# Kernel tuning notes

Measured on AMD Instinct MI355X. Metric: run time of the kernel, lower is better.

The kernel has to match this reference:

```python
import jax, jax.numpy as jnp
import numpy as np

N, E = 50000, 800000
IN, HID, OUT = 128, 128, 64
BN_EPS = 1e-5


def _w(key, fan_in, fan_out):
    return jax.random.normal(key, (fan_in, fan_out), dtype=jnp.float32) / np.sqrt(fan_in)


def setup_inputs() -> dict:
    key = jax.random.key(0)
    ks = jax.random.split(key, 12)
    x = jax.random.normal(ks[0], (N, IN), dtype=jnp.float32)
    src = jax.random.randint(ks[1], (E,), 0, N, dtype=jnp.int32)
    dst = jax.random.randint(ks[2], (E,), 0, N, dtype=jnp.int32)
    eps = jax.random.normal(ks[3], (N, OUT), dtype=jnp.float32)
    return {
        "x": x, "src": src, "dst": dst, "eps": eps,
        # SAGEConv 1: in -> hidden (lin_l has bias, lin_r no bias, mean aggr)
        "W1l": _w(ks[4], IN, HID), "W1r": _w(ks[5], IN, HID), "b1": jnp.zeros((HID,), jnp.float32),
        "g1": jnp.ones((HID,), jnp.float32), "be1": jnp.zeros((HID,), jnp.float32),
        # SAGEConv 2: hidden -> 2*hidden
        "W2l": _w(ks[6], HID, 2 * HID), "W2r": _w(ks[7], HID, 2 * HID), "b2": jnp.zeros((2 * HID,), jnp.float32),
        "g2": jnp.ones((2 * HID,), jnp.float32), "be2": jnp.zeros((2 * HID,), jnp.float32),
        # SAGEConv 3: 2*hidden -> 2*out
        "W3l": _w(ks[8], 2 * HID, 2 * OUT), "W3r": _w(ks[9], 2 * HID, 2 * OUT), "b3": jnp.zeros((2 * OUT,), jnp.float32),
    }


def _sage(h, src, dst, Wl, Wr, b):
    # mean-aggregate source features at destination nodes, then two GEMMs
    msg = jax.ops.segment_sum(h[src], dst, num_segments=N)          # [N, F]
    deg = jax.ops.segment_sum(jnp.ones((src.shape[0],), h.dtype), dst, num_segments=N)
    aggr = msg / jnp.maximum(deg, 1.0)[:, None]
    return aggr @ Wl + h @ Wr + b


def _bn(h, gamma, beta):
    m = jnp.mean(h, axis=0)
    v = jnp.var(h, axis=0)
    return gamma * (h - m) * jax.lax.rsqrt(v + BN_EPS) + beta


def reference(x, src, dst, eps, W1l, W1r, b1, g1, be1, W2l, W2r, b2, g2, be2, W3l, W3r, b3):
    h = jax.nn.relu(_sage(x, src, dst, W1l, W1r, b1))
    h = _bn(h, g1, be1)                       # dropout = identity (eval)
    h = jax.nn.relu(_sage(h, src, dst, W2l, W2r, b2))
    h = _bn(h, g2, be2)
    h = _sage(h, src, dst, W3l, W3r, b3)      # [N, 2*OUT]
    mean, log_std = jnp.split(h, 2, axis=-1)
    z = mean + jnp.exp(log_std) * eps         # reparameterize
    return z
```

## Files before the change

kernel.cpp:

```cpp
#include <hip/hip_runtime.h>
#include <math.h>

#define N_NODES 50000
#define N_EDGES 800000
#define BN_EPS_F 1e-5f
#define SCAN_BS 512
#define SCAN_NB 98
#define GXP 392

typedef unsigned short ushort_t;
typedef unsigned int uint_t;
typedef __attribute__((ext_vector_type(8))) short bf16x8;
typedef __attribute__((ext_vector_type(4))) float f32x4;

static __device__ __forceinline__ float4 ld4(const float* p) {
    return *reinterpret_cast<const float4*>(p);
}
static __device__ __forceinline__ float bf2f(ushort_t u) {
    return __uint_as_float(((uint_t)u) << 16);
}
static __device__ __forceinline__ ushort_t f2b(float f) {
    uint_t u = __float_as_uint(f);
    u += 0x7fffu + ((u >> 16) & 1u);
    return (ushort_t)(u >> 16);
}
static __device__ __forceinline__ void gload16(const void* g, void* l) {
    __builtin_amdgcn_global_load_lds(
        (const __attribute__((address_space(1))) void*)g,
        (__attribute__((address_space(3))) void*)l, 16, 0, 0);
}


__global__ void k_zero_i32(int* __restrict__ p, int n) {
    int i = blockIdx.x * blockDim.x + threadIdx.x;
    if (i < n) p[i] = 0;
}

__global__ void k_pre(const int* __restrict__ dst, int* __restrict__ deg,
                      ushort_t* __restrict__ rank,
                      const float* __restrict__ x, ushort_t* __restrict__ xb,
                      const float* __restrict__ W1l, const float* __restrict__ W1r,
                      const float* __restrict__ W2l, ushort_t* __restrict__ wt1l,
                      ushort_t* __restrict__ wt1r, ushort_t* __restrict__ wt2l) {
    int b = blockIdx.x;
    if (b < 6250) {
        int role = b & 1;
        int id = (b >> 1) * 256 + threadIdx.x;
        if (role == 0) {
            rank[id] = (ushort_t)atomicAdd(&deg[dst[id]], 1);
        } else {
            float4 a = ld4(x + (size_t)id * 8);
            float4 c = ld4(x + (size_t)id * 8 + 4);
            uint_t o0 = (uint_t)f2b(a.x) | ((uint_t)f2b(a.y) << 16);
            uint_t o1 = (uint_t)f2b(a.z) | ((uint_t)f2b(a.w) << 16);
            uint_t o2 = (uint_t)f2b(c.x) | ((uint_t)f2b(c.y) << 16);
            uint_t o3 = (uint_t)f2b(c.z) | ((uint_t)f2b(c.w) << 16);
            *reinterpret_cast<uint4*>(xb + (size_t)id * 8) = make_uint4(o0, o1, o2, o3);
        }
    } else {
        int idx = (b - 6250) * 256 + threadIdx.x;
        if (idx < 16384) {
            int f = idx >> 7, k = idx & 127;
            wt1l[idx] = f2b(W1l[(size_t)k * 128 + f]);
        } else if (idx < 32768) {
            int j = idx - 16384;
            int f = j >> 7, k = j & 127;
            wt1r[j] = f2b(W1r[(size_t)k * 128 + f]);
        } else {
            int j = idx - 32768;
            int f = j >> 7, k = j & 127;
            wt2l[j] = f2b(W2l[(size_t)k * 256 + f]);
        }
    }
}

__global__ void k_scan1(const int* __restrict__ deg, int* __restrict__ offs, int* __restrict__ bsum) {
    __shared__ int sh[SCAN_BS];
    int t = threadIdx.x;
    int g = blockIdx.x * SCAN_BS + t;
    int v = (g < N_NODES) ? deg[g] : 0;
    sh[t] = v;
    __syncthreads();
    for (int off = 1; off < SCAN_BS; off <<= 1) {
        int add = (t >= off) ? sh[t - off] : 0;
        __syncthreads();
        sh[t] += add;
        __syncthreads();
    }
    if (g < N_NODES) offs[g] = sh[t] - v;
    if (t == SCAN_BS - 1) bsum[blockIdx.x] = sh[t];
}

__global__ void k_scan2(int* __restrict__ bsum, int nb) {
    __shared__ int sh[128];
    int t = threadIdx.x;
    int v = (t < nb) ? bsum[t] : 0;
    sh[t] = v;
    __syncthreads();
    for (int off = 1; off < 128; off <<= 1) {
        int add = (t >= off) ? sh[t - off] : 0;
        __syncthreads();
        sh[t] += add;
        __syncthreads();
    }
    if (t < nb) bsum[t] = sh[t] - v;
}

__global__ void k_scan3(const int* __restrict__ deg, int* __restrict__ offs,
                        const int* __restrict__ bsum, float* __restrict__ inv_deg) {
    int g = blockIdx.x * blockDim.x + threadIdx.x;
    if (g < N_NODES) {
        offs[g] += bsum[g / SCAN_BS];
        int d = deg[g];
        inv_deg[g] = 1.0f / (float)(d > 1 ? d : 1);
    }
}

__global__ void k_fill2(const int* __restrict__ src, const int* __restrict__ dst,
                        const int* __restrict__ offs, const ushort_t* __restrict__ rank,
                        ushort_t* __restrict__ eids) {
    int e = blockIdx.x * blockDim.x + threadIdx.x;
    if (e < N_EDGES) eids[offs[dst[e]] + (int)rank[e]] = (ushort_t)src[e];
}


__global__ void k_prep2(const float* __restrict__ W2r, const float* __restrict__ b2,
                        const float* __restrict__ scsh1, ushort_t* __restrict__ wt2r,
                        float* __restrict__ bias2) {
    int bid = blockIdx.x;
    if (bid < 128) {
        int idx = bid * 256 + threadIdx.x;
        int f = idx >> 7, k = idx & 127;
        wt2r[idx] = f2b(scsh1[k] * W2r[(size_t)k * 256 + f]);
    } else {
        int f = threadIdx.x;
        float s = b2[f];
        for (int k = 0; k < 128; ++k) s += scsh1[128 + k] * W2r[(size_t)k * 256 + f];
        bias2[f] = s;
    }
}

__global__ void k_prep3(const float* __restrict__ W3l, const float* __restrict__ W3r,
                        const float* __restrict__ b3, const float* __restrict__ scsh2,
                        ushort_t* __restrict__ wt3l, ushort_t* __restrict__ wt3r,
                        float* __restrict__ bias3l, float* __restrict__ bias3r) {
    int bid = blockIdx.x;
    if (bid < 256) {
        int half = bid >> 7;
        int idx = (bid & 127) * 256 + threadIdx.x;
        int f = idx >> 8, k = idx & 255;
        const float* W = half ? W3r : W3l;
        ushort_t* WT = half ? wt3r : wt3l;
        WT[idx] = f2b(scsh2[k] * W[(size_t)k * 128 + f]);
    } else {
        int t = threadIdx.x;
        int f = t & 127;
        const float* W = (t < 128) ? W3l : W3r;
        float s = (t < 128) ? 0.f : b3[f];
        for (int k = 0; k < 256; ++k) s += scsh2[256 + k] * W[(size_t)k * 128 + f];
        float* out = (t < 128) ? bias3l : bias3r;
        out[f] = s;
    }
}


#define ACCUM8(a) do { \
    acc[0] += bf2f((ushort_t)(a).x); acc[1] += bf2f((ushort_t)((a).x >> 16)); \
    acc[2] += bf2f((ushort_t)(a).y); acc[3] += bf2f((ushort_t)((a).y >> 16)); \
    acc[4] += bf2f((ushort_t)(a).z); acc[5] += bf2f((ushort_t)((a).z >> 16)); \
    acc[6] += bf2f((ushort_t)(a).w); acc[7] += bf2f((ushort_t)((a).w >> 16)); } while (0)

static __device__ __forceinline__ void gather_rows(
        const ushort_t* __restrict__ h, const ushort_t* __restrict__ eids,
        int beg, int d, int g, size_t coff, float* acc) {
    int j = 0;
    for (; j + 32 <= d; j += 32) {
        int s[8];
#pragma unroll
        for (int k = 0; k < 8; ++k) s[k] = eids[beg + j + k * 4 + g];
        uint4 a[8];
#pragma unroll
        for (int k = 0; k < 8; ++k) a[k] = *reinterpret_cast<const uint4*>(h + (size_t)s[k] * 128 + coff);
#pragma unroll
        for (int k = 0; k < 8; ++k) ACCUM8(a[k]);
    }
    for (; j + 16 <= d; j += 16) {
        int s[4];
#pragma unroll
        for (int k = 0; k < 4; ++k) s[k] = eids[beg + j + k * 4 + g];
        uint4 a[4];
#pragma unroll
        for (int k = 0; k < 4; ++k) a[k] = *reinterpret_cast<const uint4*>(h + (size_t)s[k] * 128 + coff);
#pragma unroll
        for (int k = 0; k < 4; ++k) ACCUM8(a[k]);
    }
    for (; j + 8 <= d; j += 8) {
        int s0 = eids[beg + j + g];
        int s1 = eids[beg + j + 4 + g];
        uint4 a = *reinterpret_cast<const uint4*>(h + (size_t)s0 * 128 + coff);
        uint4 b = *reinterpret_cast<const uint4*>(h + (size_t)s1 * 128 + coff);
        ACCUM8(a); ACCUM8(b);
    }
    for (; j < d; j += 4) {
        int e = j + g;
        if (e < d) {
            int s0 = eids[beg + e];
            uint4 a = *reinterpret_cast<const uint4*>(h + (size_t)s0 * 128 + coff);
            ACCUM8(a);
        }
    }
}

template<int BN>
__global__ __launch_bounds__(256) void k_agg16(
        const ushort_t* __restrict__ h, const ushort_t* __restrict__ eids,
        const int* __restrict__ offs, const int* __restrict__ deg,
        const float* __restrict__ inv_deg, const float* __restrict__ scsh,
        ushort_t* __restrict__ out) {
    int node = (blockIdx.x * 256 + threadIdx.x) >> 6;
    int lane = threadIdx.x & 63;
    if (node >= N_NODES) return;
    const int g = lane >> 4;
    const int lr = lane & 15;
    float acc[8];
#pragma unroll
    for (int v = 0; v < 8; ++v) acc[v] = 0.f;
    const int beg = offs[node];
    const int d = deg[node];
    const size_t coff = (size_t)lr * 8;
    gather_rows(h, eids, beg, d, g, coff, acc);
#pragma unroll
    for (int v = 0; v < 8; ++v) acc[v] += __shfl_xor(acc[v], 16);
#pragma unroll
    for (int v = 0; v < 8; ++v) acc[v] += __shfl_xor(acc[v], 32);

    if (g == 0) {
        float sc = inv_deg[node];
        if (BN) {
            float4 sa0 = ld4(&scsh[lr * 8]), sa1 = ld4(&scsh[lr * 8 + 4]);
            float4 sb0 = ld4(&scsh[128 + lr * 8]), sb1 = ld4(&scsh[128 + lr * 8 + 4]);
            if (d > 0) {
                acc[0] = acc[0] * sc * sa0.x + sb0.x; acc[1] = acc[1] * sc * sa0.y + sb0.y;
                acc[2] = acc[2] * sc * sa0.z + sb0.z; acc[3] = acc[3] * sc * sa0.w + sb0.w;
                acc[4] = acc[4] * sc * sa1.x + sb1.x; acc[5] = acc[5] * sc * sa1.y + sb1.y;
                acc[6] = acc[6] * sc * sa1.z + sb1.z; acc[7] = acc[7] * sc * sa1.w + sb1.w;
            } else {
#pragma unroll
                for (int v = 0; v < 8; ++v) acc[v] = 0.f;
            }
        } else {
#pragma unroll
            for (int v = 0; v < 8; ++v) acc[v] *= sc;
        }
        uint4 o;
        o.x = (uint_t)f2b(acc[0]) | ((uint_t)f2b(acc[1]) << 16);
        o.y = (uint_t)f2b(acc[2]) | ((uint_t)f2b(acc[3]) << 16);
        o.z = (uint_t)f2b(acc[4]) | ((uint_t)f2b(acc[5]) << 16);
        o.w = (uint_t)f2b(acc[6]) | ((uint_t)f2b(acc[7]) << 16);
        *reinterpret_cast<uint4*>(out + (size_t)node * 128 + coff) = o;
    }
}

__global__ __launch_bounds__(256) void k_agg_reparam(
        const ushort_t* __restrict__ t3, const ushort_t* __restrict__ eids,
        const int* __restrict__ offs, const int* __restrict__ deg,
        const float* __restrict__ inv_deg, const float* __restrict__ u,
        const float* __restrict__ eps, float* __restrict__ z) {
    int node = (blockIdx.x * 256 + threadIdx.x) >> 6;
    int lane = threadIdx.x & 63;
    if (node >= N_NODES) return;
    const int g = lane >> 4;
    const int lr = lane & 15;
    float acc[8];
#pragma unroll
    for (int v = 0; v < 8; ++v) acc[v] = 0.f;
    const int beg = offs[node];
    const int d = deg[node];
    const size_t coff = (size_t)lr * 8;
    gather_rows(t3, eids, beg, d, g, coff, acc);
#pragma unroll
    for (int v = 0; v < 8; ++v) acc[v] += __shfl_xor(acc[v], 16);
#pragma unroll
    for (int v = 0; v < 8; ++v) acc[v] += __shfl_xor(acc[v], 32);
    float ls[8];
#pragma unroll
    for (int v = 0; v < 8; ++v) ls[v] = __shfl_down(acc[v], 8);

    if (g == 0 && lr < 8) {
        float sc = inv_deg[node];
        const float* um = u + (size_t)node * 128 + lr * 8;
        const float* ul = u + (size_t)node * 128 + 64 + lr * 8;
        const float* ep = eps + (size_t)node * 64 + lr * 8;
        float4 um0 = ld4(um), um1 = ld4(um + 4);
        float4 ul0 = ld4(ul), ul1 = ld4(ul + 4);
        float4 e0 = ld4(ep), e1 = ld4(ep + 4);
        float4 o0, o1;
        o0.x = (acc[0] * sc + um0.x) + expf(ls[0] * sc + ul0.x) * e0.x;
        o0.y = (acc[1] * sc + um0.y) + expf(ls[1] * sc + ul0.y) * e0.y;
        o0.z = (acc[2] * sc + um0.z) + expf(ls[2] * sc + ul0.z) * e0.z;
        o0.w = (acc[3] * sc + um0.w) + expf(ls[3] * sc + ul0.w) * e0.w;
        o1.x = (acc[4] * sc + um1.x) + expf(ls[4] * sc + ul1.x) * e1.x;
        o1.y = (acc[5] * sc + um1.y) + expf(ls[5] * sc + ul1.y) * e1.y;
        o1.z = (acc[6] * sc + um1.z) + expf(ls[6] * sc + ul1.z) * e1.z;
        o1.w = (acc[7] * sc + um1.w) + expf(ls[7] * sc + ul1.w) * e1.w;
        float* zp = z + (size_t)node * 64 + lr * 8;
        *reinterpret_cast<float4*>(zp) = o0;
        *reinterpret_cast<float4*>(zp + 4) = o1;
    }
}


template<int RELU, int OUTB, int DUAL, int BIAS, int STATS, int SELY>
__global__ __launch_bounds__(256) void k_gemm_mfma(
        const ushort_t* __restrict__ A1, const ushort_t* __restrict__ A2,
        const ushort_t* __restrict__ B1, const ushort_t* __restrict__ B2,
        const float* __restrict__ bias, void* __restrict__ out,
        int K, int F, float* __restrict__ partials,
        const float* __restrict__ bias2, void* __restrict__ out2) {
    __shared__ __align__(16) short lds[8192];
    const int tid = threadIdx.x;
    const int lane = tid & 63;
    const int w = tid >> 6;
    const int row0 = blockIdx.x * 128;
    const int col0 = SELY ? 0 : blockIdx.y * 128;
    const int wr = (w >> 1) * 64;
    const int wc = (w & 1) * 64;

    const ushort_t* __restrict__ B0 = (SELY && blockIdx.y) ? B2 : B1;
    const float* __restrict__ biasp = (SELY && blockIdx.y) ? bias2 : bias;
    void* __restrict__ outp = (SELY && blockIdx.y) ? out2 : out;
    const bool outb = SELY ? (blockIdx.y == 0) : (OUTB != 0);

    int rowA[2], slA[2];
#pragma unroll
    for (int p = 0; p < 2; ++p) {
        int c = (p * 4 + w) * 64 + lane;
        int r = c >> 2, sp = c & 3;
        rowA[p] = r;
        slA[p] = sp ^ ((r >> 1) & 3);
    }
    const int q = lane >> 4, lr = lane & 15;
    int aoff[4], boff[4];
#pragma unroll
    for (int f = 0; f < 4; ++f) {
        int ra = wr + f * 16 + lr;
        aoff[f] = ra * 32 + (q ^ ((ra >> 1) & 3)) * 8;
        int rb = wc + f * 16 + lr;
        boff[f] = 4096 + rb * 32 + (q ^ ((rb >> 1) & 3)) * 8;
    }

    f32x4 acc[4][4];
#pragma unroll
    for (int mf = 0; mf < 4; ++mf)
#pragma unroll
        for (int nf = 0; nf < 4; ++nf)
            acc[mf][nf] = (f32x4){0.f, 0.f, 0.f, 0.f};

    for (int m = 0; m < (DUAL ? 2 : 1); ++m) {
        const ushort_t* __restrict__ A = m ? A2 : A1;
        const ushort_t* __restrict__ B = m ? B2 : B0;
        for (int k0 = 0; k0 < K; k0 += 32) {
            __syncthreads();
#pragma unroll
            for (int p = 0; p < 2; ++p) {
                int gr = row0 + rowA[p];
                if (gr > N_NODES - 1) gr = N_NODES - 1;
                gload16(A + (size_t)gr * K + k0 + slA[p] * 8, &lds[(p * 4 + w) * 512]);
                int gc = col0 + rowA[p];
                gload16(B + (size_t)gc * K + k0 + slA[p] * 8, &lds[4096 + (p * 4 + w) * 512]);
            }
            asm volatile("s_waitcnt vmcnt(0)" ::: "memory");
            __syncthreads();
            bf16x8 av[4], bv[4];
#pragma unroll
            for (int f = 0; f < 4; ++f) {
                av[f] = *reinterpret_cast<const bf16x8*>(&lds[aoff[f]]);
                bv[f] = *reinterpret_cast<const bf16x8*>(&lds[boff[f]]);
            }
#pragma unroll
            for (int mf = 0; mf < 4; ++mf)
#pragma unroll
                for (int nf = 0; nf < 4; ++nf)
                    acc[mf][nf] = __builtin_amdgcn_mfma_f32_16x16x32_bf16(
                        av[mf], bv[nf], acc[mf][nf], 0, 0, 0);
        }
    }

    const int orow = row0 + wr + q * 4;
    const int ocol = col0 + wc + lr;
    float s[4], s2[4];
#pragma unroll
    for (int nf = 0; nf < 4; ++nf) { s[nf] = 0.f; s2[nf] = 0.f; }
#pragma unroll
    for (int nf = 0; nf < 4; ++nf) {
        int colg = ocol + nf * 16;
        float bvs = BIAS ? biasp[colg] : 0.f;
#pragma unroll
        for (int mf = 0; mf < 4; ++mf) {
#pragma unroll
            for (int b = 0; b < 4; ++b) {
                int r = orow + mf * 16 + b;
                if (r < N_NODES) {
                    float v = acc[mf][nf][b] + bvs;
                    if (RELU) v = fmaxf(v, 0.f);
                    if (STATS) { s[nf] += v; s2[nf] += v * v; }
                    if (outb)
                        ((ushort_t*)outp)[(size_t)r * F + colg] = f2b(v);
                    else
                        ((float*)outp)[(size_t)r * F + colg] = v;
                }
            }
        }
    }

    if constexpr (STATS) {
        __syncthreads();
        float* sdf = (float*)lds;
        const int u = (w >> 1) * 4 + q;
#pragma unroll
        for (int nf = 0; nf < 4; ++nf) {
            int cb = wc + nf * 16 + lr;
            sdf[u * 128 + cb] = s[nf];
            sdf[1024 + u * 128 + cb] = s2[nf];
        }
        __syncthreads();
        if (tid < 128) {
            float ss = 0.f, qq = 0.f;
#pragma unroll
            for (int u2 = 0; u2 < 8; ++u2) {
                ss += sdf[u2 * 128 + tid];
                qq += sdf[1024 + u2 * 128 + tid];
            }
            int cg = col0 + tid;
            partials[(size_t)cg * GXP + blockIdx.x] = ss;
            partials[(size_t)(F + cg) * GXP + blockIdx.x] = qq;
        }
    }
}


template<int F>
__global__ __launch_bounds__(64) void k_bn_scsh(
        const float* __restrict__ partials, const float* __restrict__ gamma,
        const float* __restrict__ beta, float* __restrict__ scsh, int GX) {
    const int c = blockIdx.x;
    const int l = threadIdx.x;
    float s = 0.f, q2 = 0.f;
    for (int g = l; g < GX; g += 64) {
        s += partials[(size_t)c * GXP + g];
        q2 += partials[(size_t)(F + c) * GXP + g];
    }
#pragma unroll
    for (int off = 1; off < 64; off <<= 1) {
        s += __shfl_xor(s, off);
        q2 += __shfl_xor(q2, off);
    }
    if (l == 0) {
        float mean = s * (1.0f / N_NODES);
        float var = q2 * (1.0f / N_NODES) - mean * mean;
        float sc = gamma[c] * rsqrtf(var + BN_EPS_F);
        scsh[c] = sc;
        scsh[F + c] = beta[c] - mean * sc;
    }
}


extern "C" void kernel_launch(void* const* d_in, const int* in_sizes, int n_in,
                              void* d_out, int out_size, void* d_ws, size_t ws_size,
                              hipStream_t stream) {
    (void)in_sizes; (void)n_in; (void)out_size; (void)ws_size;
    const float* x   = (const float*)d_in[0];
    const int*   src = (const int*)d_in[1];
    const int*   dst = (const int*)d_in[2];
    const float* eps = (const float*)d_in[3];
    const float* W1l = (const float*)d_in[4];
    const float* W1r = (const float*)d_in[5];
    const float* b1  = (const float*)d_in[6];
    const float* g1  = (const float*)d_in[7];
    const float* be1 = (const float*)d_in[8];
    const float* W2l = (const float*)d_in[9];
    const float* W2r = (const float*)d_in[10];
    const float* b2  = (const float*)d_in[11];
    const float* g2  = (const float*)d_in[12];
    const float* be2 = (const float*)d_in[13];
    const float* W3l = (const float*)d_in[14];
    const float* W3r = (const float*)d_in[15];
    const float* b3  = (const float*)d_in[16];
    float* z = (float*)d_out;

    char* ws = (char*)d_ws;
    size_t off = 0;
    auto alloc = [&](size_t bytes) -> char* {
        char* p = ws + off;
        off += (bytes + 255) & ~(size_t)255;
        return p;
    };
    int*      deg    = (int*)alloc(N_NODES * 4);
    size_t zero_bytes = off;
    ushort_t* rank   = (ushort_t*)alloc((size_t)N_EDGES * 2);
    ushort_t* eids   = (ushort_t*)alloc((size_t)N_EDGES * 2);
    float*    scshs  = (float*)alloc(1024 * 4);
    float*    biases = (float*)alloc(512 * 4);
    int*      offs   = (int*)alloc(N_NODES * 4);
    int*      bsum   = (int*)alloc(128 * 4);
    float*    invd   = (float*)alloc(N_NODES * 4);
    ushort_t* xb     = (ushort_t*)alloc((size_t)N_NODES * 128 * 2);
    ushort_t* h1b    = (ushort_t*)alloc((size_t)N_NODES * 128 * 2);
    ushort_t* h2b    = (ushort_t*)alloc((size_t)N_NODES * 256 * 2);
    ushort_t* aggrb  = (ushort_t*)alloc((size_t)N_NODES * 256 * 2);
    float*    u3f    = (float*)alloc((size_t)N_NODES * 128 * 4);
    float*    parts  = (float*)alloc((size_t)512 * GXP * 4);
    ushort_t* wt1l   = (ushort_t*)alloc(128 * 128 * 2);
    ushort_t* wt1r   = (ushort_t*)alloc(128 * 128 * 2);
    ushort_t* wt2l   = (ushort_t*)alloc(256 * 128 * 2);
    ushort_t* wt2r   = (ushort_t*)alloc(256 * 128 * 2);
    ushort_t* wt3l   = (ushort_t*)alloc(128 * 256 * 2);
    ushort_t* wt3r   = (ushort_t*)alloc(128 * 256 * 2);
    ushort_t* t3b    = aggrb;

    float* scsh1  = scshs;
    float* scsh2  = scshs + 256;
    float* bias2  = biases;
    float* bias3l = biases + 256;
    float* bias3r = biases + 384;

    k_zero_i32<<<((int)(zero_bytes / 4) + 255) / 256, 256, 0, stream>>>((int*)ws, (int)(zero_bytes / 4));
    k_pre<<<6506, 256, 0, stream>>>(dst, deg, rank, x, xb, W1l, W1r, W2l, wt1l, wt1r, wt2l);
    k_scan1<<<SCAN_NB, SCAN_BS, 0, stream>>>(deg, offs, bsum);
    k_scan2<<<1, 128, 0, stream>>>(bsum, SCAN_NB);
    k_scan3<<<(N_NODES + 255) / 256, 256, 0, stream>>>(deg, offs, bsum, invd);
    k_fill2<<<(N_EDGES + 255) / 256, 256, 0, stream>>>(src, dst, offs, rank, eids);

    const int AGG_BLKS = (N_NODES + 3) / 4;
    const int GX = (N_NODES + 127) / 128;

    k_agg16<0><<<AGG_BLKS, 256, 0, stream>>>(xb, eids, offs, deg, invd, nullptr, aggrb);
    k_gemm_mfma<1, 1, 1, 1, 1, 0><<<dim3(GX, 1), 256, 0, stream>>>(aggrb, xb, wt1l, wt1r, b1, h1b, 128, 128, parts, nullptr, nullptr);
    k_bn_scsh<128><<<128, 64, 0, stream>>>(parts, g1, be1, scsh1, GX);

    k_prep2<<<129, 256, 0, stream>>>(W2r, b2, scsh1, wt2r, bias2);
    k_agg16<1><<<AGG_BLKS, 256, 0, stream>>>(h1b, eids, offs, deg, invd, scsh1, aggrb);
    k_gemm_mfma<1, 1, 1, 1, 1, 0><<<dim3(GX, 2), 256, 0, stream>>>(aggrb, h1b, wt2l, wt2r, bias2, h2b, 128, 256, parts, nullptr, nullptr);
    k_bn_scsh<256><<<256, 64, 0, stream>>>(parts, g2, be2, scsh2, GX);

    k_prep3<<<257, 256, 0, stream>>>(W3l, W3r, b3, scsh2, wt3l, wt3r, bias3l, bias3r);
    k_gemm_mfma<0, 1, 0, 1, 0, 1><<<dim3(GX, 2), 256, 0, stream>>>(h2b, nullptr, wt3l, wt3r, bias3l, t3b, 256, 128, nullptr, bias3r, u3f);
    k_agg_reparam<<<AGG_BLKS, 256, 0, stream>>>(t3b, eids, offs, deg, invd, u3f, eps, z);
}
```

Baseline: 269.9 us.

## Gather one node per 16-lane group and store root term as bf16

```diff
diff --git a/kernel.cpp b/kernel.cpp
--- a/kernel.cpp
+++ b/kernel.cpp
@@ -170,44 +170,41 @@
     acc[4] += bf2f((ushort_t)(a).z); acc[5] += bf2f((ushort_t)((a).z >> 16)); \
     acc[6] += bf2f((ushort_t)(a).w); acc[7] += bf2f((ushort_t)((a).w >> 16)); } while (0)
 
-static __device__ __forceinline__ void gather_rows(
+static __device__ __forceinline__ void gather_rows_g(
         const ushort_t* __restrict__ h, const ushort_t* __restrict__ eids,
-        int beg, int d, int g, size_t coff, float* acc) {
+        int beg, int d, size_t coff, float* acc) {
     int j = 0;
-    for (; j + 32 <= d; j += 32) {
-        int s[8];
-#pragma unroll
-        for (int k = 0; k < 8; ++k) s[k] = eids[beg + j + k * 4 + g];
+    for (; j + 8 <= d; j += 8) {
         uint4 a[8];
 #pragma unroll
-        for (int k = 0; k < 8; ++k) a[k] = *reinterpret_cast<const uint4*>(h + (size_t)s[k] * 128 + coff);
+        for (int k = 0; k < 8; ++k) {
+            int s = eids[beg + j + k];
+            a[k] = *reinterpret_cast<const uint4*>(h + (size_t)s * 128 + coff);
+        }
 #pragma unroll
         for (int k = 0; k < 8; ++k) ACCUM8(a[k]);
     }
-    for (; j + 16 <= d; j += 16) {
-        int s[4];
-#pragma unroll
-        for (int k = 0; k < 4; ++k) s[k] = eids[beg + j + k * 4 + g];
+    for (; j + 4 <= d; j += 4) {
         uint4 a[4];
 #pragma unroll
-        for (int k = 0; k < 4; ++k) a[k] = *reinterpret_cast<const uint4*>(h + (size_t)s[k] * 128 + coff);
+        for (int k = 0; k < 4; ++k) {
+            int s = eids[beg + j + k];
+            a[k] = *reinterpret_cast<const uint4*>(h + (size_t)s * 128 + coff);
+        }
 #pragma unroll
         for (int k = 0; k < 4; ++k) ACCUM8(a[k]);
     }
-    for (; j + 8 <= d; j += 8) {
-        int s0 = eids[beg + j + g];
-        int s1 = eids[beg + j + 4 + g];
+    for (; j + 2 <= d; j += 2) {
+        int s0 = eids[beg + j];
+        int s1 = eids[beg + j + 1];
         uint4 a = *reinterpret_cast<const uint4*>(h + (size_t)s0 * 128 + coff);
         uint4 b = *reinterpret_cast<const uint4*>(h + (size_t)s1 * 128 + coff);
         ACCUM8(a); ACCUM8(b);
     }
-    for (; j < d; j += 4) {
-        int e = j + g;
-        if (e < d) {
-            int s0 = eids[beg + e];
-            uint4 a = *reinterpret_cast<const uint4*>(h + (size_t)s0 * 128 + coff);
-            ACCUM8(a);
-        }
+    if (j < d) {
+        int s0 = eids[beg + j];
+        uint4 a = *reinterpret_cast<const uint4*>(h + (size_t)s0 * 128 + coff);
+        ACCUM8(a);
     }
 }
 
@@ -217,92 +214,85 @@
         const int* __restrict__ offs, const int* __restrict__ deg,
         const float* __restrict__ inv_deg, const float* __restrict__ scsh,
         ushort_t* __restrict__ out) {
-    int node = (blockIdx.x * 256 + threadIdx.x) >> 6;
-    int lane = threadIdx.x & 63;
+    const int node = blockIdx.x * 16 + (threadIdx.x >> 4);
+    const int lr = threadIdx.x & 15;
     if (node >= N_NODES) return;
-    const int g = lane >> 4;
-    const int lr = lane & 15;
     float acc[8];
 #pragma unroll
     for (int v = 0; v < 8; ++v) acc[v] = 0.f;
     const int beg = offs[node];
     const int d = deg[node];
     const size_t coff = (size_t)lr * 8;
-    gather_rows(h, eids, beg, d, g, coff, acc);
-#pragma unroll
-    for (int v = 0; v < 8; ++v) acc[v] += __shfl_xor(acc[v], 16);
-#pragma unroll
-    for (int v = 0; v < 8; ++v) acc[v] += __shfl_xor(acc[v], 32);
-
-    if (g == 0) {
-        float sc = inv_deg[node];
-        if (BN) {
-            float4 sa0 = ld4(&scsh[lr * 8]), sa1 = ld4(&scsh[lr * 8 + 4]);
-            float4 sb0 = ld4(&scsh[128 + lr * 8]), sb1 = ld4(&scsh[128 + lr * 8 + 4]);
-            if (d > 0) {
-                acc[0] = acc[0] * sc * sa0.x + sb0.x; acc[1] = acc[1] * sc * sa0.y + sb0.y;
-                acc[2] = acc[2] * sc * sa0.z + sb0.z; acc[3] = acc[3] * sc * sa0.w + sb0.w;
-                acc[4] = acc[4] * sc * sa1.x + sb1.x; acc[5] = acc[5] * sc * sa1.y + sb1.y;
-                acc[6] = acc[6] * sc * sa1.z + sb1.z; acc[7] = acc[7] * sc * sa1.w + sb1.w;
-            } else {
-#pragma unroll
-                for (int v = 0; v < 8; ++v) acc[v] = 0.f;
-            }
+    gather_rows_g(h, eids, beg, d, coff, acc);
+
+    float sc = inv_deg[node];
+    if (BN) {
+        float4 sa0 = ld4(&scsh[lr * 8]), sa1 = ld4(&scsh[lr * 8 + 4]);
+        float4 sb0 = ld4(&scsh[128 + lr * 8]), sb1 = ld4(&scsh[128 + lr * 8 + 4]);
+        if (d > 0) {
+            acc[0] = acc[0] * sc * sa0.x + sb0.x; acc[1] = acc[1] * sc * sa0.y + sb0.y;
+            acc[2] = acc[2] * sc * sa0.z + sb0.z; acc[3] = acc[3] * sc * sa0.w + sb0.w;
+            acc[4] = acc[4] * sc * sa1.x + sb1.x; acc[5] = acc[5] * sc * sa1.y + sb1.y;
+            acc[6] = acc[6] * sc * sa1.z + sb1.z; acc[7] = acc[7] * sc * sa1.w + sb1.w;
         } else {
 #pragma unroll
-            for (int v = 0; v < 8; ++v) acc[v] *= sc;
-        }
-        uint4 o;
-        o.x = (uint_t)f2b(acc[0]) | ((uint_t)f2b(acc[1]) << 16);
-        o.y = (uint_t)f2b(acc[2]) | ((uint_t)f2b(acc[3]) << 16);
-        o.z = (uint_t)f2b(acc[4]) | ((uint_t)f2b(acc[5]) << 16);
-        o.w = (uint_t)f2b(acc[6]) | ((uint_t)f2b(acc[7]) << 16);
-        *reinterpret_cast<uint4*>(out + (size_t)node * 128 + coff) = o;
-    }
+            for (int v = 0; v < 8; ++v) acc[v] = 0.f;
+        }
+    } else {
+#pragma unroll
+        for (int v = 0; v < 8; ++v) acc[v] *= sc;
+    }
+    uint4 o;
+    o.x = (uint_t)f2b(acc[0]) | ((uint_t)f2b(acc[1]) << 16);
+    o.y = (uint_t)f2b(acc[2]) | ((uint_t)f2b(acc[3]) << 16);
+    o.z = (uint_t)f2b(acc[4]) | ((uint_t)f2b(acc[5]) << 16);
+    o.w = (uint_t)f2b(acc[6]) | ((uint_t)f2b(acc[7]) << 16);
+    *reinterpret_cast<uint4*>(out + (size_t)node * 128 + coff) = o;
 }
 
 __global__ __launch_bounds__(256) void k_agg_reparam(
         const ushort_t* __restrict__ t3, const ushort_t* __restrict__ eids,
         const int* __restrict__ offs, const int* __restrict__ deg,
-        const float* __restrict__ inv_deg, const float* __restrict__ u,
+        const float* __restrict__ inv_deg, const ushort_t* __restrict__ u,
         const float* __restrict__ eps, float* __restrict__ z) {
-    int node = (blockIdx.x * 256 + threadIdx.x) >> 6;
-    int lane = threadIdx.x & 63;
+    const int node = blockIdx.x * 16 + (threadIdx.x >> 4);
+    const int lr = threadIdx.x & 15;
     if (node >= N_NODES) return;
-    const int g = lane >> 4;
-    const int lr = lane & 15;
     float acc[8];
 #pragma unroll
     for (int v = 0; v < 8; ++v) acc[v] = 0.f;
     const int beg = offs[node];
     const int d = deg[node];
     const size_t coff = (size_t)lr * 8;
-    gather_rows(t3, eids, beg, d, g, coff, acc);
-#pragma unroll
-    for (int v = 0; v < 8; ++v) acc[v] += __shfl_xor(acc[v], 16);
-#pragma unroll
-    for (int v = 0; v < 8; ++v) acc[v] += __shfl_xor(acc[v], 32);
+    gather_rows_g(t3, eids, beg, d, coff, acc);
     float ls[8];
 #pragma unroll
     for (int v = 0; v < 8; ++v) ls[v] = __shfl_down(acc[v], 8);
 
-    if (g == 0 && lr < 8) {
+    if (lr < 8) {
         float sc = inv_deg[node];
-        const float* um = u + (size_t)node * 128 + lr * 8;
-        const float* ul = u + (size_t)node * 128 + 64 + lr * 8;
+        uint4 um4 = *reinterpret_cast<const uint4*>(u + (size_t)node * 128 + lr * 8);
+        uint4 ul4 = *reinterpret_cast<const uint4*>(u + (size_t)node * 128 + 64 + lr * 8);
         const float* ep = eps + (size_t)node * 64 + lr * 8;
-        float4 um0 = ld4(um), um1 = ld4(um + 4);
-        float4 ul0 = ld4(ul), ul1 = ld4(ul + 4);
         float4 e0 = ld4(ep), e1 = ld4(ep + 4);
+        float um[8], ul[8];
+        um[0] = bf2f((ushort_t)um4.x); um[1] = bf2f((ushort_t)(um4.x >> 16));
+        um[2] = bf2f((ushort_t)um4.y); um[3] = bf2f((ushort_t)(um4.y >> 16));
+        um[4] = bf2f((ushort_t)um4.z); um[5] = bf2f((ushort_t)(um4.z >> 16));
+        um[6] = bf2f((ushort_t)um4.w); um[7] = bf2f((ushort_t)(um4.w >> 16));
+        ul[0] = bf2f((ushort_t)ul4.x); ul[1] = bf2f((ushort_t)(ul4.x >> 16));
+        ul[2] = bf2f((ushort_t)ul4.y); ul[3] = bf2f((ushort_t)(ul4.y >> 16));
+        ul[4] = bf2f((ushort_t)ul4.z); ul[5] = bf2f((ushort_t)(ul4.z >> 16));
+        ul[6] = bf2f((ushort_t)ul4.w); ul[7] = bf2f((ushort_t)(ul4.w >> 16));
         float4 o0, o1;
-        o0.x = (acc[0] * sc + um0.x) + expf(ls[0] * sc + ul0.x) * e0.x;
-        o0.y = (acc[1] * sc + um0.y) + expf(ls[1] * sc + ul0.y) * e0.y;
-        o0.z = (acc[2] * sc + um0.z) + expf(ls[2] * sc + ul0.z) * e0.z;
-        o0.w = (acc[3] * sc + um0.w) + expf(ls[3] * sc + ul0.w) * e0.w;
-        o1.x = (acc[4] * sc + um1.x) + expf(ls[4] * sc + ul1.x) * e1.x;
-        o1.y = (acc[5] * sc + um1.y) + expf(ls[5] * sc + ul1.y) * e1.y;
-        o1.z = (acc[6] * sc + um1.z) + expf(ls[6] * sc + ul1.z) * e1.z;
-        o1.w = (acc[7] * sc + um1.w) + expf(ls[7] * sc + ul1.w) * e1.w;
+        o0.x = (acc[0] * sc + um[0]) + expf(ls[0] * sc + ul[0]) * e0.x;
+        o0.y = (acc[1] * sc + um[1]) + expf(ls[1] * sc + ul[1]) * e0.y;
+        o0.z = (acc[2] * sc + um[2]) + expf(ls[2] * sc + ul[2]) * e0.z;
+        o0.w = (acc[3] * sc + um[3]) + expf(ls[3] * sc + ul[3]) * e0.w;
+        o1.x = (acc[4] * sc + um[4]) + expf(ls[4] * sc + ul[4]) * e1.x;
+        o1.y = (acc[5] * sc + um[5]) + expf(ls[5] * sc + ul[5]) * e1.y;
+        o1.z = (acc[6] * sc + um[6]) + expf(ls[6] * sc + ul[6]) * e1.z;
+        o1.w = (acc[7] * sc + um[7]) + expf(ls[7] * sc + ul[7]) * e1.w;
         float* zp = z + (size_t)node * 64 + lr * 8;
         *reinterpret_cast<float4*>(zp) = o0;
         *reinterpret_cast<float4*>(zp + 4) = o1;
@@ -329,7 +319,6 @@
     const ushort_t* __restrict__ B0 = (SELY && blockIdx.y) ? B2 : B1;
     const float* __restrict__ biasp = (SELY && blockIdx.y) ? bias2 : bias;
     void* __restrict__ outp = (SELY && blockIdx.y) ? out2 : out;
-    const bool outb = SELY ? (blockIdx.y == 0) : (OUTB != 0);
 
     int rowA[2], slA[2];
 #pragma unroll
@@ -404,7 +393,7 @@
                     float v = acc[mf][nf][b] + bvs;
                     if (RELU) v = fmaxf(v, 0.f);
                     if (STATS) { s[nf] += v; s2[nf] += v * v; }
-                    if (outb)
+                    if (OUTB)
                         ((ushort_t*)outp)[(size_t)r * F + colg] = f2b(v);
                     else
                         ((float*)outp)[(size_t)r * F + colg] = v;
@@ -508,7 +497,7 @@
     ushort_t* h1b    = (ushort_t*)alloc((size_t)N_NODES * 128 * 2);
     ushort_t* h2b    = (ushort_t*)alloc((size_t)N_NODES * 256 * 2);
     ushort_t* aggrb  = (ushort_t*)alloc((size_t)N_NODES * 256 * 2);
-    float*    u3f    = (float*)alloc((size_t)N_NODES * 128 * 4);
+    ushort_t* u3b    = (ushort_t*)alloc((size_t)N_NODES * 128 * 2);
     float*    parts  = (float*)alloc((size_t)512 * GXP * 4);
     ushort_t* wt1l   = (ushort_t*)alloc(128 * 128 * 2);
     ushort_t* wt1r   = (ushort_t*)alloc(128 * 128 * 2);
@@ -531,7 +520,7 @@
     k_scan3<<<(N_NODES + 255) / 256, 256, 0, stream>>>(deg, offs, bsum, invd);
     k_fill2<<<(N_EDGES + 255) / 256, 256, 0, stream>>>(src, dst, offs, rank, eids);
 
-    const int AGG_BLKS = (N_NODES + 3) / 4;
+    const int AGG_BLKS = N_NODES / 16;
     const int GX = (N_NODES + 127) / 128;
 
     k_agg16<0><<<AGG_BLKS, 256, 0, stream>>>(xb, eids, offs, deg, invd, nullptr, aggrb);
@@ -544,6 +533,6 @@
     k_bn_scsh<256><<<256, 64, 0, stream>>>(parts, g2, be2, scsh2, GX);
 
     k_prep3<<<257, 256, 0, stream>>>(W3l, W3r, b3, scsh2, wt3l, wt3r, bias3l, bias3r);
-    k_gemm_mfma<0, 1, 0, 1, 0, 1><<<dim3(GX, 2), 256, 0, stream>>>(h2b, nullptr, wt3l, wt3r, bias3l, t3b, 256, 128, nullptr, bias3r, u3f);
-    k_agg_reparam<<<AGG_BLKS, 256, 0, stream>>>(t3b, eids, offs, deg, invd, u3f, eps, z);
-}
+    k_gemm_mfma<0, 1, 0, 1, 0, 1><<<dim3(GX, 2), 256, 0, stream>>>(h2b, nullptr, wt3l, wt3r, bias3l, t3b, 256, 128, nullptr, bias3r, u3b);
+    k_agg_reparam<<<AGG_BLKS, 256, 0, stream>>>(t3b, eids, offs, deg, invd, u3b, eps, z);
+}
```

Result: faster. 258.1 us (-4.4%).
